# Kernel tuning notes

Hardware: AMD Instinct MI355X
Metric: run time of the kernel (lower is better)

Reference implementation:

```python
import jax, jax.numpy as jnp
import numpy as np

N = 16384
INPUT_DIM = 256
HIDDEN1 = 128
HIDDEN2 = 64


def setup_inputs() -> dict:
    key = jax.random.key(0)
    ks = jax.random.split(key, 8)
    X = jax.random.normal(ks[0], (N, INPUT_DIM), dtype=jnp.float32)
    adj = jax.random.uniform(ks[1], (N, N), dtype=jnp.float32)
    # Xavier-uniform style scaling for weights
    def xavier(k, shape):
        fan_in, fan_out = shape
        lim = float(np.sqrt(6.0 / (fan_in + fan_out)))
        return jax.random.uniform(k, shape, dtype=jnp.float32, minval=-lim, maxval=lim)
    W1 = xavier(ks[2], (INPUT_DIM, HIDDEN1))
    Wm = xavier(ks[3], (HIDDEN1, HIDDEN2))
    Ws = xavier(ks[4], (HIDDEN1, HIDDEN2))
    Wp = xavier(ks[5], (HIDDEN2, HIDDEN2))
    bp = jnp.zeros((HIDDEN2,), dtype=jnp.float32)
    noise = jax.random.normal(ks[6], (N, HIDDEN2), dtype=jnp.float32)
    return {"X": X, "adj": adj, "W1": W1, "Wm": Wm, "Ws": Ws,
            "Wp": Wp, "bp": bp, "noise": noise}


def _gcn(x, adj, W, activation):
    # GraphConvSparse: adj @ (x @ W) then activation
    h = adj @ (x @ W)
    return activation(h)


def reference(X, adj, W1, Wm, Ws, Wp, bp, noise):
    # base GCN with ReLU
    hidden = _gcn(X, adj, W1, jax.nn.relu)            # [N, hidden1]
    # mean branch: identity-activation GCN then Linear projection
    Z = _gcn(hidden, adj, Wm, lambda x: x)            # [N, hidden2]
    mean = Z @ Wp + bp                                # [N, hidden2]
    # logstd branch with clamp(max=10)
    logstd = _gcn(hidden, adj, Ws, lambda x: x)
    logstd = jnp.minimum(logstd, 10.0)
    # reparameterization trick
    sampled_z = noise * jnp.exp(logstd) + mean        # [N, hidden2]
    return sampled_z
```

## Files before the change

### kernel.cpp

```cpp
#include <hip/hip_runtime.h>


typedef __bf16 bf16_t;
typedef __attribute__((ext_vector_type(4))) __bf16 bf16x4;
typedef __attribute__((ext_vector_type(8))) __bf16 bf16x8;
typedef __attribute__((ext_vector_type(16))) float f32x16;
typedef __attribute__((ext_vector_type(4)))  float f32x4;

#define N_NODES 16384

__device__ __forceinline__ int frag_off(int r, int c) {
    int K16  = r >> 4;
    int cblk = c >> 5;
    int g    = (r >> 3) & 1;
    int lane = (c & 31) + (g << 5);
    return ((K16 * 4 + cblk) << 9) + (lane << 3) + (r & 7);
}

template<int K, bool FUSED>
__global__ __launch_bounds__(256)
void producer_kernel(const float* __restrict__ A,
                     const float* __restrict__ W,
                     const float* __restrict__ Wa,
                     const float* __restrict__ Wb,
                     bf16_t* __restrict__ Bh,
                     bf16_t* __restrict__ Bl)
{
    __shared__ float As[32][128];
    __shared__ float Wsh[32][128];
    const int t    = threadIdx.x;
    const int row0 = blockIdx.x * 128;
    const int tc   = t & 15, tr = t >> 4;

    float acc[8][8];
    #pragma unroll
    for (int i = 0; i < 8; ++i)
        #pragma unroll
        for (int j = 0; j < 8; ++j) acc[i][j] = 0.f;

    const int ra = t >> 1, ks = (t & 1) << 4;
    const int wk = t >> 3, wc = (t & 7) << 4;

    for (int k0 = 0; k0 < K; k0 += 32) {
        const float* ap = A + (size_t)(row0 + ra) * K + k0 + ks;
        float4 a0 = *(const float4*)(ap);
        float4 a1 = *(const float4*)(ap + 4);
        float4 a2 = *(const float4*)(ap + 8);
        float4 a3 = *(const float4*)(ap + 12);
        float4 w0, w1, w2, w3;
        if (!FUSED) {
            const float* wp = W + (size_t)(k0 + wk) * 128 + wc;
            w0 = *(const float4*)(wp);     w1 = *(const float4*)(wp + 4);
            w2 = *(const float4*)(wp + 8); w3 = *(const float4*)(wp + 12);
        } else {
            const float* wp = (wc < 64) ? (Wa + (size_t)(k0 + wk) * 64 + wc)
                                        : (Wb + (size_t)(k0 + wk) * 64 + (wc - 64));
            w0 = *(const float4*)(wp);     w1 = *(const float4*)(wp + 4);
            w2 = *(const float4*)(wp + 8); w3 = *(const float4*)(wp + 12);
        }
        __syncthreads();
        {
            float tmp[16] = {a0.x,a0.y,a0.z,a0.w, a1.x,a1.y,a1.z,a1.w,
                             a2.x,a2.y,a2.z,a2.w, a3.x,a3.y,a3.z,a3.w};
            #pragma unroll
            for (int j = 0; j < 16; ++j) As[ks + j][ra] = tmp[j];
            *(float4*)&Wsh[wk][wc     ] = w0;
            *(float4*)&Wsh[wk][wc +  4] = w1;
            *(float4*)&Wsh[wk][wc +  8] = w2;
            *(float4*)&Wsh[wk][wc + 12] = w3;
        }
        __syncthreads();
        #pragma unroll 4
        for (int k = 0; k < 32; ++k) {
            float av[8], wv[8];
            *(float4*)&av[0] = *(const float4*)&As[k][8 * tr];
            *(float4*)&av[4] = *(const float4*)&As[k][8 * tr + 4];
            *(float4*)&wv[0] = *(const float4*)&Wsh[k][8 * tc];
            *(float4*)&wv[4] = *(const float4*)&Wsh[k][8 * tc + 4];
            #pragma unroll
            for (int i = 0; i < 8; ++i)
                #pragma unroll
                for (int j = 0; j < 8; ++j)
                    acc[i][j] = fmaf(av[i], wv[j], acc[i][j]);
        }
    }

    #pragma unroll
    for (int i = 0; i < 8; ++i) {
        int r = row0 + 8 * tr + i;
        #pragma unroll
        for (int j = 0; j < 8; ++j) {
            int c = 8 * tc + j;
            float v = acc[i][j];
            bf16_t h = (bf16_t)v;
            bf16_t l = (bf16_t)(v - (float)h);
            int off = frag_off(r, c);
            Bh[off] = h;
            Bl[off] = l;
        }
    }
}

template<int ACT>
__global__ __launch_bounds__(512, 2)
void adj_gemm_kernel(const float* __restrict__ adj,
                     const bf16_t* __restrict__ Bh,
                     const bf16_t* __restrict__ Bl,
                     float* __restrict__ out)
{
    __shared__ __align__(16) bf16_t AsH[2][64 * 256];
    __shared__ __align__(16) bf16_t AsL[2][64 * 256];
    const int t    = threadIdx.x;
    const int lane = t & 63;
    const int w    = t >> 6;
    const int wr   = w >> 2, wc = w & 3;
    const int row0 = blockIdx.x * 64;

    const float* aBase = adj + (size_t)(row0 + w * 8) * 16384 + lane * 4;

    const int frow = (wr << 5) + (lane & 31);
    const int fg   = (lane >> 5) << 3;
    const int rswz = (frow & 7) << 3;
    const int rbase = frow << 8;

    const int tb = (wc << 9) + (lane << 3);

    f32x16 acc;
    #pragma unroll
    for (int i = 0; i < 16; ++i) acc[i] = 0.f;

    f32x4 ar[8];

    auto loadAdj = [&](int mac) {
        const float* p = aBase + (mac << 8);
        ar[0] = __builtin_nontemporal_load((const f32x4*)(p));
        ar[1] = __builtin_nontemporal_load((const f32x4*)(p + 16384));
        ar[2] = __builtin_nontemporal_load((const f32x4*)(p + 2 * 16384));
        ar[3] = __builtin_nontemporal_load((const f32x4*)(p + 3 * 16384));
        ar[4] = __builtin_nontemporal_load((const f32x4*)(p + 4 * 16384));
        ar[5] = __builtin_nontemporal_load((const f32x4*)(p + 5 * 16384));
        ar[6] = __builtin_nontemporal_load((const f32x4*)(p + 6 * 16384));
        ar[7] = __builtin_nontemporal_load((const f32x4*)(p + 7 * 16384));
    };
    auto cvtWrite = [&](int buf) {
        #pragma unroll
        for (int j = 0; j < 8; ++j) {
            bf16x4 hv, lv;
            #pragma unroll
            for (int e = 0; e < 4; ++e) {
                float v = ar[j][e];
                bf16_t h = (bf16_t)v;
                hv[e] = h;
                lv[e] = (bf16_t)(v - (float)h);
            }
            int idx = (((w << 3) + j) << 8) + ((lane << 2) ^ (j << 3));
            *(bf16x4*)&AsH[buf][idx] = hv;
            *(bf16x4*)&AsL[buf][idx] = lv;
        }
    };
    auto loadB = [&](bf16x8* bh, bf16x8* bl, int sub) {
        const size_t base = ((size_t)sub << 13) + tb;
        #pragma unroll
        for (int s = 0; s < 4; ++s) {
            bh[s] = *(const bf16x8*)(Bh + base + (s << 11));
            bl[s] = *(const bf16x8*)(Bl + base + (s << 11));
        }
    };
    auto compute = [&](int buf, const bf16x8* bh, const bf16x8* bl, int sbase) {
        #pragma unroll
        for (int s = 0; s < 4; ++s) {
            int idx = rbase + ((((sbase + s) << 4) + fg) ^ rswz);
            bf16x8 ah = *(const bf16x8*)&AsH[buf][idx];
            bf16x8 al = *(const bf16x8*)&AsL[buf][idx];
            acc = __builtin_amdgcn_mfma_f32_32x32x16_bf16(ah, bh[s], acc, 0, 0, 0);
            acc = __builtin_amdgcn_mfma_f32_32x32x16_bf16(ah, bl[s], acc, 0, 0, 0);
            acc = __builtin_amdgcn_mfma_f32_32x32x16_bf16(al, bh[s], acc, 0, 0, 0);
        }
    };

#define SYNC_LDS() do { asm volatile("s_waitcnt lgkmcnt(0)" ::: "memory"); \
                        __builtin_amdgcn_s_barrier(); } while (0)

    bf16x8 bhS0[4], blS0[4], bhS1[4], blS1[4];
    bf16x8 bhS2[4], blS2[4], bhS3[4], blS3[4];

    loadAdj(0);
    cvtWrite(0);
    loadB(bhS0, blS0, 0);
    loadB(bhS1, blS1, 1);
    SYNC_LDS();
    loadAdj(1);

    for (int m = 0; m < 63; ++m) {
        const int buf = m & 1;
        const int s4 = m << 2;
        loadB(bhS2, blS2, s4 + 2);
        compute(buf, bhS0, blS0, 0);
        loadB(bhS3, blS3, s4 + 3);
        compute(buf, bhS1, blS1, 4);
        loadB(bhS0, blS0, s4 + 4);
        cvtWrite(buf ^ 1);
        compute(buf, bhS2, blS2, 8);
        loadB(bhS1, blS1, s4 + 5);
        compute(buf, bhS3, blS3, 12);
        SYNC_LDS();
        if (m < 62) loadAdj(m + 2);
    }
    loadB(bhS2, blS2, 254);
    compute(1, bhS0, blS0, 0);
    loadB(bhS3, blS3, 255);
    compute(1, bhS1, blS1, 4);
    compute(1, bhS2, blS2, 8);
    compute(1, bhS3, blS3, 12);
#undef SYNC_LDS

    const int col = (wc << 5) + (lane & 31);
    const int rb  = row0 + (wr << 5) + ((lane >> 5) << 2);
    #pragma unroll
    for (int q = 0; q < 16; ++q) {
        int r = rb + (q & 3) + ((q >> 2) << 3);
        float v = acc[q];
        if (ACT == 1) v = fmaxf(v, 0.f);
        out[(size_t)r * 128 + col] = v;
    }
}

__global__ __launch_bounds__(256)
void final_kernel(const float* __restrict__ T,
                  const float* __restrict__ Wp,
                  const float* __restrict__ bp,
                  const float* __restrict__ noise,
                  float* __restrict__ out)
{
    __shared__ float Wps[64][64];
    __shared__ float Ts[64][64];
    const int t = threadIdx.x;
    const int row0 = blockIdx.x * 64;
    {
        int k = t >> 2, c0 = (t & 3) << 4;
        #pragma unroll
        for (int i = 0; i < 4; ++i)
            *(float4*)&Wps[k][c0 + 4 * i] = *(const float4*)&Wp[(size_t)k * 64 + c0 + 4 * i];
        #pragma unroll
        for (int i = 0; i < 4; ++i)
            *(float4*)&Ts[k][c0 + 4 * i] =
                *(const float4*)&T[(size_t)(row0 + k) * 128 + c0 + 4 * i];
    }
    __syncthreads();

    const int r  = t >> 2;
    const int c0 = (t & 3) << 4;
    float acc[16];
    #pragma unroll
    for (int j = 0; j < 16; ++j) acc[j] = bp[c0 + j];
    for (int k = 0; k < 64; ++k) {
        float a = Ts[r][k];
        #pragma unroll
        for (int j = 0; j < 16; ++j) acc[j] = fmaf(a, Wps[k][c0 + j], acc[j]);
    }
    const int grow = row0 + r;
    #pragma unroll
    for (int j = 0; j < 16; ++j) {
        float ls = T[(size_t)grow * 128 + 64 + c0 + j];
        ls = fminf(ls, 10.0f);
        out[(size_t)grow * 64 + c0 + j] =
            noise[(size_t)grow * 64 + c0 + j] * __expf(ls) + acc[j];
    }
}

extern "C" void kernel_launch(void* const* d_in, const int* in_sizes, int n_in,
                              void* d_out, int out_size, void* d_ws, size_t ws_size,
                              hipStream_t stream) {
    const float* X     = (const float*)d_in[0];
    const float* adj   = (const float*)d_in[1];
    const float* W1    = (const float*)d_in[2];
    const float* Wm    = (const float*)d_in[3];
    const float* Wsv   = (const float*)d_in[4];
    const float* Wp    = (const float*)d_in[5];
    const float* bp    = (const float*)d_in[6];
    const float* noise = (const float*)d_in[7];
    float* out = (float*)d_out;

    char* ws = (char*)d_ws;
    bf16_t* Bh   = (bf16_t*)ws;
    bf16_t* Bl   = (bf16_t*)(ws + (4u << 20));
    float*  Htmp = (float*)(ws + (8u << 20));

    producer_kernel<256, false><<<128, 256, 0, stream>>>(X, W1, nullptr, nullptr, Bh, Bl);
    adj_gemm_kernel<1><<<256, 512, 0, stream>>>(adj, Bh, Bl, Htmp);
    producer_kernel<128, true><<<128, 256, 0, stream>>>(Htmp, nullptr, Wm, Wsv, Bh, Bl);
    adj_gemm_kernel<0><<<256, 512, 0, stream>>>(adj, Bh, Bl, Htmp);
    final_kernel<<<256, 256, 0, stream>>>(Htmp, Wp, bp, noise, out);
}
```

Before: 724.6 us.

## Use 128-row tiles with split-K halves in adj GEMM, reducing partials downstream

The adj GEMM now uses 128-row tiles, with each wave computing two 32x32 accumulators so every B fragment load feeds twice as many MFMAs. To keep the same 256 blocks, the K dimension is split in two halves, and each half writes its own fp32 partial buffer. The downstream producer and final kernels add the two partials, and ReLU moves into the producer. This halves B-operand traffic per adj element but adds extra partial-buffer reads and writes, and raises register pressure.

Result: slower. 1.270 ms (+75.2%).

```diff
diff --git a/kernel.cpp b/kernel.cpp
--- a/kernel.cpp
+++ b/kernel.cpp
@@ -2,10 +2,10 @@
 
 
 typedef __bf16 bf16_t;
-typedef __attribute__((ext_vector_type(4))) __bf16 bf16x4;
+typedef __attribute__((ext_vector_type(2))) __bf16 bf16x2;
 typedef __attribute__((ext_vector_type(8))) __bf16 bf16x8;
 typedef __attribute__((ext_vector_type(16))) float f32x16;
-typedef __attribute__((ext_vector_type(4)))  float f32x4;
+typedef __attribute__((ext_vector_type(2)))  float f32x2;
 
 #define N_NODES 16384
 
@@ -17,9 +17,17 @@
     return ((K16 * 4 + cblk) << 9) + (lane << 3) + (r & 7);
 }
 
-template<int K, bool FUSED>
+__device__ __forceinline__ float4 relu_add4(float4 a, float4 b) {
+    float4 r;
+    r.x = fmaxf(a.x + b.x, 0.f); r.y = fmaxf(a.y + b.y, 0.f);
+    r.z = fmaxf(a.z + b.z, 0.f); r.w = fmaxf(a.w + b.w, 0.f);
+    return r;
+}
+
+template<int K, bool FUSED, bool ADD2>
 __global__ __launch_bounds__(256)
 void producer_kernel(const float* __restrict__ A,
+                     const float* __restrict__ A2,
                      const float* __restrict__ W,
                      const float* __restrict__ Wa,
                      const float* __restrict__ Wb,
@@ -47,6 +55,13 @@
         float4 a1 = *(const float4*)(ap + 4);
         float4 a2 = *(const float4*)(ap + 8);
         float4 a3 = *(const float4*)(ap + 12);
+        if (ADD2) {
+            const float* ap2 = A2 + (size_t)(row0 + ra) * K + k0 + ks;
+            a0 = relu_add4(a0, *(const float4*)(ap2));
+            a1 = relu_add4(a1, *(const float4*)(ap2 + 4));
+            a2 = relu_add4(a2, *(const float4*)(ap2 + 8));
+            a3 = relu_add4(a3, *(const float4*)(ap2 + 12));
+        }
         float4 w0, w1, w2, w3;
         if (!FUSED) {
             const float* wp = W + (size_t)(k0 + wk) * 128 + wc;
@@ -101,132 +116,143 @@
     }
 }
 
-template<int ACT>
+struct BSet { bf16x8 h[4]; bf16x8 l[4]; };
+
 __global__ __launch_bounds__(512, 2)
 void adj_gemm_kernel(const float* __restrict__ adj,
                      const bf16_t* __restrict__ Bh,
                      const bf16_t* __restrict__ Bl,
-                     float* __restrict__ out)
+                     float* __restrict__ P0,
+                     float* __restrict__ P1)
 {
-    __shared__ __align__(16) bf16_t AsH[2][64 * 256];
-    __shared__ __align__(16) bf16_t AsL[2][64 * 256];
+    __shared__ __align__(16) bf16_t AsH[2][128 * 128];
+    __shared__ __align__(16) bf16_t AsL[2][128 * 128];
     const int t    = threadIdx.x;
     const int lane = t & 63;
     const int w    = t >> 6;
     const int wr   = w >> 2, wc = w & 3;
-    const int row0 = blockIdx.x * 64;
-
-    const float* aBase = adj + (size_t)(row0 + w * 8) * 16384 + lane * 4;
-
-    const int frow = (wr << 5) + (lane & 31);
-    const int fg   = (lane >> 5) << 3;
-    const int rswz = (frow & 7) << 3;
-    const int rbase = frow << 8;
-
-    const int tb = (wc << 9) + (lane << 3);
-
-    f32x16 acc;
-    #pragma unroll
-    for (int i = 0; i < 16; ++i) acc[i] = 0.f;
-
-    f32x4 ar[8];
+    const int mt   = blockIdx.x >> 1;
+    const int kh   = blockIdx.x & 1;
+    const int row0 = mt << 7;
+    float* const outP = kh ? P1 : P0;
+
+    const float* aBase = adj + (size_t)(row0 + (w << 4)) * 16384
+                             + ((size_t)kh << 13) + (lane << 1);
+
+    const int frow0 = (wr << 6) + (lane & 31);
+    const int fg    = (lane >> 5) << 3;
+    const int sw    = (frow0 & 15) << 3;
+    const int rb0   = frow0 << 7;
+    const int rb1   = (frow0 + 32) << 7;
+
+    const int tb   = (wc << 9) + (lane << 3);
+    const int khs  = kh << 7;
+
+    f32x16 acc0, acc1;
+    #pragma unroll
+    for (int i = 0; i < 16; ++i) { acc0[i] = 0.f; acc1[i] = 0.f; }
+
+    f32x2 ar[16];
 
     auto loadAdj = [&](int mac) {
-        const float* p = aBase + (mac << 8);
-        ar[0] = __builtin_nontemporal_load((const f32x4*)(p));
-        ar[1] = __builtin_nontemporal_load((const f32x4*)(p + 16384));
-        ar[2] = __builtin_nontemporal_load((const f32x4*)(p + 2 * 16384));
-        ar[3] = __builtin_nontemporal_load((const f32x4*)(p + 3 * 16384));
-        ar[4] = __builtin_nontemporal_load((const f32x4*)(p + 4 * 16384));
-        ar[5] = __builtin_nontemporal_load((const f32x4*)(p + 5 * 16384));
-        ar[6] = __builtin_nontemporal_load((const f32x4*)(p + 6 * 16384));
-        ar[7] = __builtin_nontemporal_load((const f32x4*)(p + 7 * 16384));
+        const float* p = aBase + (mac << 7);
+        #pragma unroll
+        for (int j = 0; j < 16; ++j)
+            ar[j] = __builtin_nontemporal_load((const f32x2*)(p + (size_t)j * 16384));
     };
     auto cvtWrite = [&](int buf) {
-        #pragma unroll
-        for (int j = 0; j < 8; ++j) {
-            bf16x4 hv, lv;
-            #pragma unroll
-            for (int e = 0; e < 4; ++e) {
-                float v = ar[j][e];
-                bf16_t h = (bf16_t)v;
-                hv[e] = h;
-                lv[e] = (bf16_t)(v - (float)h);
-            }
-            int idx = (((w << 3) + j) << 8) + ((lane << 2) ^ (j << 3));
-            *(bf16x4*)&AsH[buf][idx] = hv;
-            *(bf16x4*)&AsL[buf][idx] = lv;
+        bf16_t* const H = buf ? &AsH[1][0] : &AsH[0][0];
+        bf16_t* const L = buf ? &AsL[1][0] : &AsL[0][0];
+        #pragma unroll
+        for (int j = 0; j < 16; ++j) {
+            const int r = (w << 4) + j;
+            const int idx = (r << 7) + ((lane << 1) ^ (j << 3));
+            float v0 = ar[j][0], v1 = ar[j][1];
+            bf16_t h0 = (bf16_t)v0, h1 = (bf16_t)v1;
+            bf16x2 hv = {h0, h1};
+            bf16x2 lv = {(bf16_t)(v0 - (float)h0), (bf16_t)(v1 - (float)h1)};
+            *(bf16x2*)&H[idx] = hv;
+            *(bf16x2*)&L[idx] = lv;
         }
     };
-    auto loadB = [&](bf16x8* bh, bf16x8* bl, int sub) {
-        const size_t base = ((size_t)sub << 13) + tb;
+    auto loadB = [&](BSet& S, int sub) {
+        const size_t base = ((size_t)(khs + sub) << 13) + tb;
         #pragma unroll
         for (int s = 0; s < 4; ++s) {
-            bh[s] = *(const bf16x8*)(Bh + base + (s << 11));
-            bl[s] = *(const bf16x8*)(Bl + base + (s << 11));
+            S.h[s] = *(const bf16x8*)(Bh + base + (s << 11));
+            S.l[s] = *(const bf16x8*)(Bl + base + (s << 11));
         }
     };
-    auto compute = [&](int buf, const bf16x8* bh, const bf16x8* bl, int sbase) {
+    auto computeHalf = [&](int buf, const BSet& S, int half) {
+        const bf16_t* const H = buf ? &AsH[1][0] : &AsH[0][0];
+        const bf16_t* const L = buf ? &AsL[1][0] : &AsL[0][0];
         #pragma unroll
         for (int s = 0; s < 4; ++s) {
-            int idx = rbase + ((((sbase + s) << 4) + fg) ^ rswz);
-            bf16x8 ah = *(const bf16x8*)&AsH[buf][idx];
-            bf16x8 al = *(const bf16x8*)&AsL[buf][idx];
-            acc = __builtin_amdgcn_mfma_f32_32x32x16_bf16(ah, bh[s], acc, 0, 0, 0);
-            acc = __builtin_amdgcn_mfma_f32_32x32x16_bf16(ah, bl[s], acc, 0, 0, 0);
-            acc = __builtin_amdgcn_mfma_f32_32x32x16_bf16(al, bh[s], acc, 0, 0, 0);
+            const int o = ((((half << 2) + s) << 4) + fg) ^ sw;
+            bf16x8 ah0 = *(const bf16x8*)&H[rb0 + o];
+            bf16x8 al0 = *(const bf16x8*)&L[rb0 + o];
+            bf16x8 ah1 = *(const bf16x8*)&H[rb1 + o];
+            bf16x8 al1 = *(const bf16x8*)&L[rb1 + o];
+            acc0 = __builtin_amdgcn_mfma_f32_32x32x16_bf16(ah0, S.h[s], acc0, 0, 0, 0);
+            acc0 = __builtin_amdgcn_mfma_f32_32x32x16_bf16(ah0, S.l[s], acc0, 0, 0, 0);
+            acc0 = __builtin_amdgcn_mfma_f32_32x32x16_bf16(al0, S.h[s], acc0, 0, 0, 0);
+            acc1 = __builtin_amdgcn_mfma_f32_32x32x16_bf16(ah1, S.h[s], acc1, 0, 0, 0);
+            acc1 = __builtin_amdgcn_mfma_f32_32x32x16_bf16(ah1, S.l[s], acc1, 0, 0, 0);
+            acc1 = __builtin_amdgcn_mfma_f32_32x32x16_bf16(al1, S.h[s], acc1, 0, 0, 0);
         }
     };
 
 #define SYNC_LDS() do { asm volatile("s_waitcnt lgkmcnt(0)" ::: "memory"); \
                         __builtin_amdgcn_s_barrier(); } while (0)
 
-    bf16x8 bhS0[4], blS0[4], bhS1[4], blS1[4];
-    bf16x8 bhS2[4], blS2[4], bhS3[4], blS3[4];
+    BSet S0, S1, S2, S3;
 
     loadAdj(0);
+    loadB(S0, 0);
+    loadB(S1, 1);
     cvtWrite(0);
-    loadB(bhS0, blS0, 0);
-    loadB(bhS1, blS1, 1);
     SYNC_LDS();
     loadAdj(1);
 
-    for (int m = 0; m < 63; ++m) {
-        const int buf = m & 1;
-        const int s4 = m << 2;
-        loadB(bhS2, blS2, s4 + 2);
-        compute(buf, bhS0, blS0, 0);
-        loadB(bhS3, blS3, s4 + 3);
-        compute(buf, bhS1, blS1, 4);
-        loadB(bhS0, blS0, s4 + 4);
-        cvtWrite(buf ^ 1);
-        compute(buf, bhS2, blS2, 8);
-        loadB(bhS1, blS1, s4 + 5);
-        compute(buf, bhS3, blS3, 12);
+    for (int m = 0; m < 62; m += 2) {
+        loadB(S2, 2 * m + 2);
+        computeHalf(0, S0, 0);
+        loadB(S3, 2 * m + 3);
+        computeHalf(0, S1, 1);
+        cvtWrite(1);
         SYNC_LDS();
-        if (m < 62) loadAdj(m + 2);
-    }
-    loadB(bhS2, blS2, 254);
-    compute(1, bhS0, blS0, 0);
-    loadB(bhS3, blS3, 255);
-    compute(1, bhS1, blS1, 4);
-    compute(1, bhS2, blS2, 8);
-    compute(1, bhS3, blS3, 12);
+        loadAdj(m + 2);
+        loadB(S0, 2 * m + 4);
+        computeHalf(1, S2, 0);
+        loadB(S1, 2 * m + 5);
+        computeHalf(1, S3, 1);
+        cvtWrite(0);
+        SYNC_LDS();
+        loadAdj(m + 3);
+    }
+    loadB(S2, 126);
+    computeHalf(0, S0, 0);
+    loadB(S3, 127);
+    computeHalf(0, S1, 1);
+    cvtWrite(1);
+    SYNC_LDS();
+    computeHalf(1, S2, 0);
+    computeHalf(1, S3, 1);
 #undef SYNC_LDS
 
     const int col = (wc << 5) + (lane & 31);
-    const int rb  = row0 + (wr << 5) + ((lane >> 5) << 2);
+    const int rw  = row0 + (wr << 6) + ((lane >> 5) << 2);
     #pragma unroll
     for (int q = 0; q < 16; ++q) {
-        int r = rb + (q & 3) + ((q >> 2) << 3);
-        float v = acc[q];
-        if (ACT == 1) v = fmaxf(v, 0.f);
-        out[(size_t)r * 128 + col] = v;
+        int r = rw + (q & 3) + ((q >> 2) << 3);
+        outP[(size_t)r * 128 + col] = acc0[q];
+        outP[(size_t)(r + 32) * 128 + col] = acc1[q];
     }
 }
 
 __global__ __launch_bounds__(256)
-void final_kernel(const float* __restrict__ T,
+void final_kernel(const float* __restrict__ T0,
+                  const float* __restrict__ T1,
                   const float* __restrict__ Wp,
                   const float* __restrict__ bp,
                   const float* __restrict__ noise,
@@ -242,9 +268,13 @@
         for (int i = 0; i < 4; ++i)
             *(float4*)&Wps[k][c0 + 4 * i] = *(const float4*)&Wp[(size_t)k * 64 + c0 + 4 * i];
         #pragma unroll
-        for (int i = 0; i < 4; ++i)
-            *(float4*)&Ts[k][c0 + 4 * i] =
-                *(const float4*)&T[(size_t)(row0 + k) * 128 + c0 + 4 * i];
+        for (int i = 0; i < 4; ++i) {
+            float4 z0 = *(const float4*)&T0[(size_t)(row0 + k) * 128 + c0 + 4 * i];
+            float4 z1 = *(const float4*)&T1[(size_t)(row0 + k) * 128 + c0 + 4 * i];
+            float4 zs; zs.x = z0.x + z1.x; zs.y = z0.y + z1.y;
+            zs.z = z0.z + z1.z; zs.w = z0.w + z1.w;
+            *(float4*)&Ts[k][c0 + 4 * i] = zs;
+        }
     }
     __syncthreads();
 
@@ -261,7 +291,8 @@
     const int grow = row0 + r;
     #pragma unroll
     for (int j = 0; j < 16; ++j) {
-        float ls = T[(size_t)grow * 128 + 64 + c0 + j];
+        size_t li = (size_t)grow * 128 + 64 + c0 + j;
+        float ls = T0[li] + T1[li];
         ls = fminf(ls, 10.0f);
         out[(size_t)grow * 64 + c0 + j] =
             noise[(size_t)grow * 64 + c0 + j] * __expf(ls) + acc[j];
@@ -282,13 +313,16 @@
     float* out = (float*)d_out;
 
     char* ws = (char*)d_ws;
-    bf16_t* Bh   = (bf16_t*)ws;
-    bf16_t* Bl   = (bf16_t*)(ws + (4u << 20));
-    float*  Htmp = (float*)(ws + (8u << 20));
-
-    producer_kernel<256, false><<<128, 256, 0, stream>>>(X, W1, nullptr, nullptr, Bh, Bl);
-    adj_gemm_kernel<1><<<256, 512, 0, stream>>>(adj, Bh, Bl, Htmp);
-    producer_kernel<128, true><<<128, 256, 0, stream>>>(Htmp, nullptr, Wm, Wsv, Bh, Bl);
-    adj_gemm_kernel<0><<<256, 512, 0, stream>>>(adj, Bh, Bl, Htmp);
-    final_kernel<<<256, 256, 0, stream>>>(Htmp, Wp, bp, noise, out);
-}
+    bf16_t* Bh = (bf16_t*)ws;
+    bf16_t* Bl = (bf16_t*)(ws + (4u << 20));
+    float*  P0 = (float*)(ws + (8u << 20));
+    float*  P1 = (float*)(ws + (16u << 20));
+
+    producer_kernel<256, false, false><<<128, 256, 0, stream>>>(
+        X, nullptr, W1, nullptr, nullptr, Bh, Bl);
+    adj_gemm_kernel<<<256, 512, 0, stream>>>(adj, Bh, Bl, P0, P1);
+    producer_kernel<128, true, true><<<128, 256, 0, stream>>>(
+        P0, P1, nullptr, Wm, Wsv, Bh, Bl);
+    adj_gemm_kernel<<<256, 512, 0, stream>>>(adj, Bh, Bl, P0, P1);
+    final_kernel<<<256, 256, 0, stream>>>(P0, P1, Wp, bp, noise, out);
+}
```

## Warp-specialize adj GEMM into producer and MFMA consumer waves

Applied to the files above, without the earlier changes.

Splits the eight waves of the adjacency GEMM into four producer waves and four consumer waves. Producers stream adj rows (16 rows each), split them into bf16 hi/lo parts and write them to LDS. Consumers load the B fragments and run the split-bf16 MFMAs into two accumulators, each covering 64 output columns. The aim is to overlap the global-memory streaming and conversion with MFMA work, instead of having every wave interleave both. The cost is higher register pressure from the larger per-wave tiles, and launch_bounds no longer requests two blocks per CU.

Result: slower. 1.115 ms (+53.8%).

```diff
diff --git a/kernel.cpp b/kernel.cpp
--- a/kernel.cpp
+++ b/kernel.cpp
@@ -8,6 +8,8 @@
 typedef __attribute__((ext_vector_type(4)))  float f32x4;
 
 #define N_NODES 16384
+#define MFMA3(ACC, A, B) \
+    ACC = __builtin_amdgcn_mfma_f32_32x32x16_bf16(A, B, ACC, 0, 0, 0)
 
 __device__ __forceinline__ int frag_off(int r, int c) {
     int K16  = r >> 4;
@@ -102,7 +104,7 @@
 }
 
 template<int ACT>
-__global__ __launch_bounds__(512, 2)
+__global__ __launch_bounds__(512)
 void adj_gemm_kernel(const float* __restrict__ adj,
                      const bf16_t* __restrict__ Bh,
                      const bf16_t* __restrict__ Bl,
@@ -113,38 +115,24 @@
     const int t    = threadIdx.x;
     const int lane = t & 63;
     const int w    = t >> 6;
-    const int wr   = w >> 2, wc = w & 3;
+    const bool prod = (w < 4);
     const int row0 = blockIdx.x * 64;
 
-    const float* aBase = adj + (size_t)(row0 + w * 8) * 16384 + lane * 4;
-
-    const int frow = (wr << 5) + (lane & 31);
-    const int fg   = (lane >> 5) << 3;
-    const int rswz = (frow & 7) << 3;
-    const int rbase = frow << 8;
-
-    const int tb = (wc << 9) + (lane << 3);
-
-    f32x16 acc;
-    #pragma unroll
-    for (int i = 0; i < 16; ++i) acc[i] = 0.f;
-
-    f32x4 ar[8];
+    const int pw = w & 3;
+    const float* aBase = adj + (size_t)(row0 + pw * 16) * 16384 + lane * 4;
+    f32x4 ar[16];
 
     auto loadAdj = [&](int mac) {
-        const float* p = aBase + (mac << 8);
-        ar[0] = __builtin_nontemporal_load((const f32x4*)(p));
-        ar[1] = __builtin_nontemporal_load((const f32x4*)(p + 16384));
-        ar[2] = __builtin_nontemporal_load((const f32x4*)(p + 2 * 16384));
-        ar[3] = __builtin_nontemporal_load((const f32x4*)(p + 3 * 16384));
-        ar[4] = __builtin_nontemporal_load((const f32x4*)(p + 4 * 16384));
-        ar[5] = __builtin_nontemporal_load((const f32x4*)(p + 5 * 16384));
-        ar[6] = __builtin_nontemporal_load((const f32x4*)(p + 6 * 16384));
-        ar[7] = __builtin_nontemporal_load((const f32x4*)(p + 7 * 16384));
+        const float* p = aBase + ((size_t)mac << 8);
+        #pragma unroll
+        for (int j = 0; j < 16; ++j)
+            ar[j] = __builtin_nontemporal_load((const f32x4*)(p + (size_t)j * 16384));
     };
     auto cvtWrite = [&](int buf) {
-        #pragma unroll
-        for (int j = 0; j < 8; ++j) {
+        bf16_t* const H = buf ? &AsH[1][0] : &AsH[0][0];
+        bf16_t* const L = buf ? &AsL[1][0] : &AsL[0][0];
+        #pragma unroll
+        for (int j = 0; j < 16; ++j) {
             bf16x4 hv, lv;
             #pragma unroll
             for (int e = 0; e < 4; ++e) {
@@ -153,75 +141,101 @@
                 hv[e] = h;
                 lv[e] = (bf16_t)(v - (float)h);
             }
-            int idx = (((w << 3) + j) << 8) + ((lane << 2) ^ (j << 3));
-            *(bf16x4*)&AsH[buf][idx] = hv;
-            *(bf16x4*)&AsL[buf][idx] = lv;
+            const int idx = ((pw * 16 + j) << 8) + ((lane << 2) ^ (j << 3));
+            *(bf16x4*)&H[idx] = hv;
+            *(bf16x4*)&L[idx] = lv;
         }
     };
-    auto loadB = [&](bf16x8* bh, bf16x8* bl, int sub) {
-        const size_t base = ((size_t)sub << 13) + tb;
+
+    const int cw   = w & 3;
+    const int cwr  = cw >> 1;
+    const int cwc  = cw & 1;
+    const int frow = (cwr << 5) + (lane & 31);
+    const int fg   = (lane >> 5) << 3;
+    const int rswz = (frow & 15) << 3;
+    const int rbase = frow << 8;
+    const int q0   = cwc << 1;
+    const int tbA  = (q0 << 9) + (lane << 3);
+    const int tbB  = ((q0 + 1) << 9) + (lane << 3);
+
+    f32x16 acc0, acc1;
+    #pragma unroll
+    for (int i = 0; i < 16; ++i) { acc0[i] = 0.f; acc1[i] = 0.f; }
+
+    struct Pair { bf16x8 ha[4], la[4], hb[4], lb[4]; };
+    Pair P0, P1;
+
+    auto loadP = [&](Pair& P, int sub) {
+        const size_t s0 = ((size_t)sub << 13);
         #pragma unroll
         for (int s = 0; s < 4; ++s) {
-            bh[s] = *(const bf16x8*)(Bh + base + (s << 11));
-            bl[s] = *(const bf16x8*)(Bl + base + (s << 11));
+            P.ha[s] = *(const bf16x8*)(Bh + s0 + tbA + (s << 11));
+            P.la[s] = *(const bf16x8*)(Bl + s0 + tbA + (s << 11));
+            P.hb[s] = *(const bf16x8*)(Bh + s0 + tbB + (s << 11));
+            P.lb[s] = *(const bf16x8*)(Bl + s0 + tbB + (s << 11));
         }
     };
-    auto compute = [&](int buf, const bf16x8* bh, const bf16x8* bl, int sbase) {
+    auto computeSub = [&](int buf, const Pair& P, int sbase) {
+        const bf16_t* const H = buf ? &AsH[1][0] : &AsH[0][0];
+        const bf16_t* const L = buf ? &AsL[1][0] : &AsL[0][0];
         #pragma unroll
         for (int s = 0; s < 4; ++s) {
-            int idx = rbase + ((((sbase + s) << 4) + fg) ^ rswz);
-            bf16x8 ah = *(const bf16x8*)&AsH[buf][idx];
-            bf16x8 al = *(const bf16x8*)&AsL[buf][idx];
-            acc = __builtin_amdgcn_mfma_f32_32x32x16_bf16(ah, bh[s], acc, 0, 0, 0);
-            acc = __builtin_amdgcn_mfma_f32_32x32x16_bf16(ah, bl[s], acc, 0, 0, 0);
-            acc = __builtin_amdgcn_mfma_f32_32x32x16_bf16(al, bh[s], acc, 0, 0, 0);
+            const int o = ((((sbase + s) << 4) + fg) ^ rswz);
+            bf16x8 ah = *(const bf16x8*)&H[rbase + o];
+            bf16x8 al = *(const bf16x8*)&L[rbase + o];
+            MFMA3(acc0, ah, P.ha[s]);
+            MFMA3(acc1, ah, P.hb[s]);
+            MFMA3(acc0, ah, P.la[s]);
+            MFMA3(acc1, ah, P.lb[s]);
+            MFMA3(acc0, al, P.ha[s]);
+            MFMA3(acc1, al, P.hb[s]);
         }
     };
 
 #define SYNC_LDS() do { asm volatile("s_waitcnt lgkmcnt(0)" ::: "memory"); \
                         __builtin_amdgcn_s_barrier(); } while (0)
 
-    bf16x8 bhS0[4], blS0[4], bhS1[4], blS1[4];
-    bf16x8 bhS2[4], blS2[4], bhS3[4], blS3[4];
-
-    loadAdj(0);
-    cvtWrite(0);
-    loadB(bhS0, blS0, 0);
-    loadB(bhS1, blS1, 1);
+    if (prod) {
+        loadAdj(0);
+        cvtWrite(0);
+        loadAdj(1);
+    } else {
+        loadP(P0, 0);
+        loadP(P1, 1);
+    }
     SYNC_LDS();
-    loadAdj(1);
 
     for (int m = 0; m < 63; ++m) {
-        const int buf = m & 1;
-        const int s4 = m << 2;
-        loadB(bhS2, blS2, s4 + 2);
-        compute(buf, bhS0, blS0, 0);
-        loadB(bhS3, blS3, s4 + 3);
-        compute(buf, bhS1, blS1, 4);
-        loadB(bhS0, blS0, s4 + 4);
-        cvtWrite(buf ^ 1);
-        compute(buf, bhS2, blS2, 8);
-        loadB(bhS1, blS1, s4 + 5);
-        compute(buf, bhS3, blS3, 12);
+        if (prod) {
+            cvtWrite((m + 1) & 1);
+            if (m < 62) loadAdj(m + 2);
+        } else {
+            const int buf = m & 1, s4 = m << 2;
+            computeSub(buf, P0, 0);   loadP(P0, s4 + 2);
+            computeSub(buf, P1, 4);   loadP(P1, s4 + 3);
+            computeSub(buf, P0, 8);   loadP(P0, s4 + 4);
+            computeSub(buf, P1, 12);  loadP(P1, s4 + 5);
+        }
         SYNC_LDS();
-        if (m < 62) loadAdj(m + 2);
-    }
-    loadB(bhS2, blS2, 254);
-    compute(1, bhS0, blS0, 0);
-    loadB(bhS3, blS3, 255);
-    compute(1, bhS1, blS1, 4);
-    compute(1, bhS2, blS2, 8);
-    compute(1, bhS3, blS3, 12);
+    }
 #undef SYNC_LDS
 
-    const int col = (wc << 5) + (lane & 31);
-    const int rb  = row0 + (wr << 5) + ((lane >> 5) << 2);
-    #pragma unroll
-    for (int q = 0; q < 16; ++q) {
-        int r = rb + (q & 3) + ((q >> 2) << 3);
-        float v = acc[q];
-        if (ACT == 1) v = fmaxf(v, 0.f);
-        out[(size_t)r * 128 + col] = v;
+    if (!prod) {
+        computeSub(1, P0, 0);   loadP(P0, 254);
+        computeSub(1, P1, 4);   loadP(P1, 255);
+        computeSub(1, P0, 8);
+        computeSub(1, P1, 12);
+
+        const int col0 = (q0 << 5) + (lane & 31);
+        const int rw   = row0 + (cwr << 5) + ((lane >> 5) << 2);
+        #pragma unroll
+        for (int q = 0; q < 16; ++q) {
+            int r = rw + (q & 3) + ((q >> 2) << 3);
+            float v0 = acc0[q], v1 = acc1[q];
+            if (ACT == 1) { v0 = fmaxf(v0, 0.f); v1 = fmaxf(v1, 0.f); }
+            out[(size_t)r * 128 + col0]      = v0;
+            out[(size_t)r * 128 + col0 + 32] = v1;
+        }
     }
 }
 
```

## Halve adj K-tile to 128 and double-buffer adjacency registers in GEMM pipeline

Applied to the files above, without the earlier changes.

Shrinks each adjacency LDS stage from 256 to 128 K-columns, halving LDS use, and adds a second register buffer for the adjacency loads so the next tile's global loads are issued two stages ahead. The LDS layout and swizzle are changed to a 16-unit XOR pattern with precomputed read and write indices. This is meant to keep more HBM loads in flight and overlap conversion with MFMA work. In exchange it doubles the number of barriers and raises register pressure at 2 blocks per CU.

New measurement: 768.3 us. 6.0% more time.

```diff
diff --git a/kernel.cpp b/kernel.cpp
--- a/kernel.cpp
+++ b/kernel.cpp
@@ -8,6 +8,8 @@
 typedef __attribute__((ext_vector_type(4)))  float f32x4;
 
 #define N_NODES 16384
+#define MFMA3(ACC, A, B) \
+    ACC = __builtin_amdgcn_mfma_f32_32x32x16_bf16(A, B, ACC, 0, 0, 0)
 
 __device__ __forceinline__ int frag_off(int r, int c) {
     int K16  = r >> 4;
@@ -101,6 +103,8 @@
     }
 }
 
+struct BSet { bf16x8 h[4]; bf16x8 l[4]; };
+
 template<int ACT>
 __global__ __launch_bounds__(512, 2)
 void adj_gemm_kernel(const float* __restrict__ adj,
@@ -108,20 +112,30 @@
                      const bf16_t* __restrict__ Bl,
                      float* __restrict__ out)
 {
-    __shared__ __align__(16) bf16_t AsH[2][64 * 256];
-    __shared__ __align__(16) bf16_t AsL[2][64 * 256];
+    __shared__ __align__(16) bf16_t AsH[2][64 * 128];
+    __shared__ __align__(16) bf16_t AsL[2][64 * 128];
     const int t    = threadIdx.x;
     const int lane = t & 63;
     const int w    = t >> 6;
     const int wr   = w >> 2, wc = w & 3;
     const int row0 = blockIdx.x * 64;
-
-    const float* aBase = adj + (size_t)(row0 + w * 8) * 16384 + lane * 4;
+    const int hi32 = lane >> 5;
+
+    const float* aBase = adj + (size_t)(row0 + w * 8 + hi32) * 16384
+                             + (lane & 31) * 4;
+    int wIdx[4];
+    #pragma unroll
+    for (int j = 0; j < 4; ++j) {
+        int row  = w * 8 + 2 * j + hi32;
+        int unit = (lane & 31) >> 1;
+        wIdx[j] = (row << 7) + ((unit ^ (row & 15)) << 3) + ((lane & 1) << 2);
+    }
 
     const int frow = (wr << 5) + (lane & 31);
-    const int fg   = (lane >> 5) << 3;
-    const int rswz = (frow & 7) << 3;
-    const int rbase = frow << 8;
+    int rIdx[8];
+    #pragma unroll
+    for (int s = 0; s < 8; ++s)
+        rIdx[s] = (frow << 7) + (((2 * s + hi32) ^ (frow & 15)) << 3);
 
     const int tb = (wc << 9) + (lane << 3);
 
@@ -129,22 +143,20 @@
     #pragma unroll
     for (int i = 0; i < 16; ++i) acc[i] = 0.f;
 
-    f32x4 ar[8];
-
-    auto loadAdj = [&](int mac) {
-        const float* p = aBase + (mac << 8);
-        ar[0] = __builtin_nontemporal_load((const f32x4*)(p));
-        ar[1] = __builtin_nontemporal_load((const f32x4*)(p + 16384));
-        ar[2] = __builtin_nontemporal_load((const f32x4*)(p + 2 * 16384));
-        ar[3] = __builtin_nontemporal_load((const f32x4*)(p + 3 * 16384));
-        ar[4] = __builtin_nontemporal_load((const f32x4*)(p + 4 * 16384));
-        ar[5] = __builtin_nontemporal_load((const f32x4*)(p + 5 * 16384));
-        ar[6] = __builtin_nontemporal_load((const f32x4*)(p + 6 * 16384));
-        ar[7] = __builtin_nontemporal_load((const f32x4*)(p + 7 * 16384));
+    f32x4 arA[4], arB[4];
+    BSet E0, E1, O0, O1;
+
+    auto loadAdj = [&](f32x4* ar, int mac) {
+        const float* p = aBase + (mac << 7);
+        #pragma unroll
+        for (int j = 0; j < 4; ++j)
+            ar[j] = __builtin_nontemporal_load((const f32x4*)(p + (size_t)j * 32768));
     };
-    auto cvtWrite = [&](int buf) {
-        #pragma unroll
-        for (int j = 0; j < 8; ++j) {
+    auto cvtWrite = [&](int buf, const f32x4* ar) {
+        bf16_t* const H = buf ? &AsH[1][0] : &AsH[0][0];
+        bf16_t* const L = buf ? &AsL[1][0] : &AsL[0][0];
+        #pragma unroll
+        for (int j = 0; j < 4; ++j) {
             bf16x4 hv, lv;
             #pragma unroll
             for (int e = 0; e < 4; ++e) {
@@ -153,69 +165,71 @@
                 hv[e] = h;
                 lv[e] = (bf16_t)(v - (float)h);
             }
-            int idx = (((w << 3) + j) << 8) + ((lane << 2) ^ (j << 3));
-            *(bf16x4*)&AsH[buf][idx] = hv;
-            *(bf16x4*)&AsL[buf][idx] = lv;
+            *(bf16x4*)&H[wIdx[j]] = hv;
+            *(bf16x4*)&L[wIdx[j]] = lv;
         }
     };
-    auto loadB = [&](bf16x8* bh, bf16x8* bl, int sub) {
+    auto loadB = [&](BSet& S, int sub) {
         const size_t base = ((size_t)sub << 13) + tb;
         #pragma unroll
         for (int s = 0; s < 4; ++s) {
-            bh[s] = *(const bf16x8*)(Bh + base + (s << 11));
-            bl[s] = *(const bf16x8*)(Bl + base + (s << 11));
+            S.h[s] = *(const bf16x8*)(Bh + base + (s << 11));
+            S.l[s] = *(const bf16x8*)(Bl + base + (s << 11));
         }
     };
-    auto compute = [&](int buf, const bf16x8* bh, const bf16x8* bl, int sbase) {
+    auto compute = [&](int buf, const BSet& S, int sbase) {
+        const bf16_t* const H = buf ? &AsH[1][0] : &AsH[0][0];
+        const bf16_t* const L = buf ? &AsL[1][0] : &AsL[0][0];
         #pragma unroll
         for (int s = 0; s < 4; ++s) {
-            int idx = rbase + ((((sbase + s) << 4) + fg) ^ rswz);
-            bf16x8 ah = *(const bf16x8*)&AsH[buf][idx];
-            bf16x8 al = *(const bf16x8*)&AsL[buf][idx];
-            acc = __builtin_amdgcn_mfma_f32_32x32x16_bf16(ah, bh[s], acc, 0, 0, 0);
-            acc = __builtin_amdgcn_mfma_f32_32x32x16_bf16(ah, bl[s], acc, 0, 0, 0);
-            acc = __builtin_amdgcn_mfma_f32_32x32x16_bf16(al, bh[s], acc, 0, 0, 0);
+            const int id = rIdx[sbase + s];
+            bf16x8 ah = *(const bf16x8*)&H[id];
+            bf16x8 al = *(const bf16x8*)&L[id];
+            MFMA3(acc, ah, S.h[s]);
+            MFMA3(acc, ah, S.l[s]);
+            MFMA3(acc, al, S.h[s]);
         }
     };
 
 #define SYNC_LDS() do { asm volatile("s_waitcnt lgkmcnt(0)" ::: "memory"); \
                         __builtin_amdgcn_s_barrier(); } while (0)
 
-    bf16x8 bhS0[4], blS0[4], bhS1[4], blS1[4];
-    bf16x8 bhS2[4], blS2[4], bhS3[4], blS3[4];
-
-    loadAdj(0);
-    cvtWrite(0);
-    loadB(bhS0, blS0, 0);
-    loadB(bhS1, blS1, 1);
+    loadB(E0, 0);
+    loadB(E1, 1);
+    loadAdj(arA, 0);
+    loadAdj(arB, 1);
+    cvtWrite(0, arA);
     SYNC_LDS();
-    loadAdj(1);
-
-    for (int m = 0; m < 63; ++m) {
-        const int buf = m & 1;
-        const int s4 = m << 2;
-        loadB(bhS2, blS2, s4 + 2);
-        compute(buf, bhS0, blS0, 0);
-        loadB(bhS3, blS3, s4 + 3);
-        compute(buf, bhS1, blS1, 4);
-        loadB(bhS0, blS0, s4 + 4);
-        cvtWrite(buf ^ 1);
-        compute(buf, bhS2, blS2, 8);
-        loadB(bhS1, blS1, s4 + 5);
-        compute(buf, bhS3, blS3, 12);
+
+    for (int m = 0; m < 126; m += 2) {
+        loadB(O0, 2 * m + 2);
+        loadB(O1, 2 * m + 3);
+        loadAdj(arA, m + 2);
+        compute(0, E0, 0);
+        compute(0, E1, 4);
+        cvtWrite(1, arB);
         SYNC_LDS();
-        if (m < 62) loadAdj(m + 2);
-    }
-    loadB(bhS2, blS2, 254);
-    compute(1, bhS0, blS0, 0);
-    loadB(bhS3, blS3, 255);
-    compute(1, bhS1, blS1, 4);
-    compute(1, bhS2, blS2, 8);
-    compute(1, bhS3, blS3, 12);
+
+        loadB(E0, 2 * m + 4);
+        loadB(E1, 2 * m + 5);
+        loadAdj(arB, m + 3);
+        compute(1, O0, 0);
+        compute(1, O1, 4);
+        cvtWrite(0, arA);
+        SYNC_LDS();
+    }
+    loadB(O0, 254);
+    loadB(O1, 255);
+    compute(0, E0, 0);
+    compute(0, E1, 4);
+    cvtWrite(1, arB);
+    SYNC_LDS();
+    compute(1, O0, 0);
+    compute(1, O1, 4);
 #undef SYNC_LDS
 
     const int col = (wc << 5) + (lane & 31);
-    const int rb  = row0 + (wr << 5) + ((lane >> 5) << 2);
+    const int rb  = row0 + (wr << 5) + (hi32 << 2);
     #pragma unroll
     for (int q = 0; q < 16; ++q) {
         int r = rb + (q & 3) + ((q >> 2) << 3);
```
